# Performance work log

Hardware: AMD Instinct MI355X
Metric: run time of the kernel (lower is better)

The kernel has to match this reference:

```python
import jax, jax.numpy as jnp
import numpy as np

D_MODEL = 768
EXPAND = 2
D_STATE = 128
HEADDIM = 64
D_CONV = 4
D_INNER = EXPAND * D_MODEL            # 1536
NHEADS = D_INNER // HEADDIM           # 24
CONV_DIM = D_INNER + 2 * D_STATE      # 1792
D_IN_PROJ = 2 * D_INNER + 2 * D_STATE + NHEADS  # 3352
EPS = 1e-5
BATCH, SEQLEN = 2, 2048


def silu(v):
    return v * jax.nn.sigmoid(v)


def mamba2(x, in_w, conv_w, conv_b, dt_bias, A_log, Dp, norm_w, out_w):
    # x: (b, l, d_model)
    b, l, _ = x.shape
    zxbcdt = x @ in_w.T                              # (b, l, d_in_proj)
    z = zxbcdt[..., :D_INNER]
    xBC = zxbcdt[..., D_INNER:D_INNER + CONV_DIM]
    dt = jax.nn.softplus(zxbcdt[..., D_INNER + CONV_DIM:] + dt_bias)  # (b, l, h)
    # causal depthwise conv1d, kernel D_CONV, left padding D_CONV-1
    pad = jnp.pad(xBC, ((0, 0), (D_CONV - 1, 0), (0, 0)))
    conv = conv_b
    for k in range(D_CONV):
        conv = conv + pad[:, k:k + l, :] * conv_w[:, k]
    xBC = silu(conv)
    xh = xBC[..., :D_INNER].reshape(b, l, NHEADS, HEADDIM)   # (b,l,h,p)
    Bm = xBC[..., D_INNER:D_INNER + D_STATE]                 # (b,l,n) ngroups=1
    Cm = xBC[..., D_INNER + D_STATE:]                        # (b,l,n)
    A = -jnp.exp(A_log)                                      # (h,)
    dA = jnp.exp(dt * A)                                     # (b,l,h)

    def step(h, inp):
        dA_t, dt_t, x_t, B_t, C_t = inp
        # h: (b, h, p, n)
        h = h * dA_t[:, :, None, None] + (dt_t[:, :, None] * x_t)[..., None] * B_t[:, None, None, :]
        y = jnp.einsum('bhpn,bn->bhp', h, C_t)
        return h, y

    h0 = jnp.zeros((b, NHEADS, HEADDIM, D_STATE), x.dtype)
    xs = (dA.transpose(1, 0, 2), dt.transpose(1, 0, 2), xh.transpose(1, 0, 2, 3),
          Bm.transpose(1, 0, 2), Cm.transpose(1, 0, 2))
    _, ys = jax.lax.scan(step, h0, xs)                       # (l,b,h,p)
    y = ys.transpose(1, 0, 2, 3) + Dp[None, None, :, None] * xh
    y = y.reshape(b, l, D_INNER)
    # RMSNormGated (norm_before_gate=False): rmsnorm(y * silu(z)) * weight
    y = y * silu(z)
    y = y * jax.lax.rsqrt(jnp.mean(jnp.square(y), axis=-1, keepdims=True) + EPS) * norm_w
    return y @ out_w.T


def setup_inputs() -> dict:
    key = jax.random.key(0)
    ks = jax.random.split(key, 9)
    s = 0.02
    return {
        'x': jax.random.normal(ks[0], (BATCH, SEQLEN, D_MODEL), jnp.float32),
        'in_proj_w': jax.random.normal(ks[1], (2, D_IN_PROJ, D_MODEL), jnp.float32) * s,
        'conv_w': jax.random.normal(ks[2], (2, CONV_DIM, D_CONV), jnp.float32) * 0.2,
        'conv_b': jax.random.normal(ks[3], (2, CONV_DIM), jnp.float32) * s,
        'dt_bias': jax.random.normal(ks[4], (2, NHEADS), jnp.float32) * 0.1,
        'A_log': jnp.log(jax.random.uniform(ks[5], (2, NHEADS), jnp.float32, 1.0, 16.0)),
        'D': jax.random.normal(ks[6], (2, NHEADS), jnp.float32) * 0.5 + 1.0,
        'norm_w': jnp.ones((2, D_INNER), jnp.float32),
        'out_proj_w': jax.random.normal(ks[7], (2, D_MODEL, D_INNER), jnp.float32) * s,
    }


def reference(x, in_proj_w, conv_w, conv_b, dt_bias, A_log, D, norm_w, out_proj_w):
    h_fwd = mamba2(x, in_proj_w[0], conv_w[0], conv_b[0], dt_bias[0], A_log[0], D[0], norm_w[0], out_proj_w[0])
    x_rev = jnp.flip(x, axis=1)
    h_bwd_rev = mamba2(x_rev, in_proj_w[1], conv_w[1], conv_b[1], dt_bias[1], A_log[1], D[1], norm_w[1], out_proj_w[1])
    return h_fwd + jnp.flip(h_bwd_rev, axis=1)
```

## Files before the change

kernel.cpp:

```cpp
#include <hip/hip_runtime.h>
#include <hip/hip_bf16.h>

typedef __attribute__((ext_vector_type(8))) short short8;
typedef __attribute__((ext_vector_type(4))) short bfx4;
typedef __attribute__((ext_vector_type(4))) float floatx4;

#define SEQ     2048
#define DMODEL  768
#define DINNER  1536
#define DSTATE  128
#define NH      24
#define CONVDIM 1792
#define NPROJ   3352
#define QCH     64
#define NCH     (SEQ / QCH)

__device__ inline float bf2f(short s) {
    return __uint_as_float(((unsigned)(unsigned short)s) << 16);
}
__device__ inline short f2bf(float f) {
    __hip_bfloat16 h = __float2bfloat16(f);
    return *reinterpret_cast<short*>(&h);
}
__device__ inline void gl_lds16(const void* g, void* l) {
    __builtin_amdgcn_global_load_lds((const __attribute__((address_space(1))) unsigned int*)g,
                                     (__attribute__((address_space(3))) unsigned int*)l, 16, 0, 0);
}

__global__ __launch_bounds__(256) void cvt_kernel(const float* __restrict__ src,
                                                  __hip_bfloat16* __restrict__ dst, int n4) {
    int i = blockIdx.x * 256 + threadIdx.x;
    if (i >= n4) return;
    float4 v = *(const float4*)(src + (size_t)i * 4);
    bfx4 o = { f2bf(v.x), f2bf(v.y), f2bf(v.z), f2bf(v.w) };
    *(bfx4*)((short*)dst + (size_t)i * 4) = o;
}

__global__ __launch_bounds__(256) void gemm_bt(const __hip_bfloat16* __restrict__ Abase, size_t aStride,
                                               const __hip_bfloat16* __restrict__ Bbase, size_t bStride,
                                               float* __restrict__ C,
                                               __hip_bfloat16* __restrict__ Zb,
                                               __hip_bfloat16* __restrict__ Xb,
                                               float* __restrict__ DT,
                                               float* __restrict__ LA,
                                               const float* __restrict__ dtbias,
                                               const float* __restrict__ Alog,
                                               int M, int N, int K, int zdiv, int mode, int flipA) {
    __shared__ short As[2][64 * 64];
    __shared__ short Bs[2][64 * 64];
    int tid = threadIdx.x;
    int w = tid >> 6, lane = tid & 63;
    int q = lane >> 4, mm = lane & 15;
    int wm = w >> 1, wn = w & 1;
    int m0 = blockIdx.x * 128, n0 = blockIdx.y * 128;
    int z = blockIdx.z;
    int dir = z / zdiv, ks = z - dir * zdiv;
    int kl = K / zdiv;
    int kbeg = ks * kl;
    const short* Ag = (const short*)Abase + (size_t)dir * aStride;
    const short* Bg = (const short*)Bbase + (size_t)dir * bStride;
    int fA = flipA && dir;

    size_t aoff[2], boff[2];
    int ldso[2];
#pragma unroll
    for (int j = 0; j < 2; j++) {
        int widx = w * 2 + j;
        int ln = widx * 8 + (lane >> 3);
        int s  = lane & 7;
        int c  = s ^ (ln & 7);
        int row = (c < 4) ? ln : ln + 64;
        int ch  = (c < 4) ? c : (c ^ 4);
        int ar = m0 + row;
        if (fA) { int bb = ar >> 11, tt = ar & 2047; ar = (bb << 11) + (2047 - tt); }
        aoff[j] = (size_t)ar * K + ch * 8;
        int br = n0 + row; if (br > N - 1) br = N - 1;
        boff[j] = (size_t)br * K + ch * 8;
        ldso[j] = widx * 1024;
    }

    floatx4 acc[16];
#pragma unroll
    for (int i = 0; i < 16; i++) acc[i] = (floatx4){0.f, 0.f, 0.f, 0.f};

    int niter = kl / 32;
    auto stage = [&](int buf, int k0) {
#pragma unroll
        for (int j = 0; j < 2; j++) {
            gl_lds16(Ag + aoff[j] + kbeg + k0, (char*)&As[buf][0] + ldso[j]);
            gl_lds16(Bg + boff[j] + kbeg + k0, (char*)&Bs[buf][0] + ldso[j]);
        }
    };
    stage(0, 0);
    int slotA = (q ^ (mm & 7) ^ (wm << 2)) * 8;
    int slotB = (q ^ (mm & 7) ^ (wn << 2)) * 8;
    for (int it = 0; it < niter; it++) {
        __syncthreads();
        if (it + 1 < niter) stage((it + 1) & 1, (it + 1) * 32);
        const short* Ab = &As[it & 1][0];
        const short* Bb = &Bs[it & 1][0];
        short8 af[4], bfr[4];
#pragma unroll
        for (int mb = 0; mb < 4; mb++)
            af[mb] = *(const short8*)&Ab[(mb * 16 + mm) * 64 + slotA];
#pragma unroll
        for (int nb = 0; nb < 4; nb++)
            bfr[nb] = *(const short8*)&Bb[(nb * 16 + mm) * 64 + slotB];
#pragma unroll
        for (int mb = 0; mb < 4; mb++)
#pragma unroll
            for (int nb = 0; nb < 4; nb++)
                acc[mb * 4 + nb] = __builtin_amdgcn_mfma_f32_16x16x32_bf16(af[mb], bfr[nb], acc[mb * 4 + nb], 0, 0, 0);
    }

    __hip_bfloat16* Zb2 = Zb + (size_t)dir * 4096 * DINNER;
    __hip_bfloat16* Xb2 = Xb + (size_t)dir * 4096 * CONVDIM;
    float* DT2 = DT + (size_t)dir * 4096 * NH;
    float* LA2 = LA + (size_t)dir * 4096 * NH;
    const float* dtb2 = dtbias + dir * NH;
    const float* Al2  = Alog + dir * NH;

#pragma unroll
    for (int mb = 0; mb < 4; mb++) {
#pragma unroll
        for (int nb = 0; nb < 4; nb++) {
            int col = n0 + wn * 64 + nb * 16 + mm;
            if (col >= N) continue;
#pragma unroll
            for (int r = 0; r < 4; r++) {
                int rr = m0 + wm * 64 + mb * 16 + q * 4 + r;
                float v = acc[mb * 4 + nb][r];
                if (mode == 1) {
                    int orow = rr;
                    if (dir) { int b = rr >> 11, t = rr & 2047; orow = (b << 11) + (2047 - t); }
                    atomicAdd(&C[(size_t)orow * N + col], v);
                } else {
                    if (col < DINNER) {
                        Zb2[(size_t)rr * DINNER + col] = __float2bfloat16(v);
                    } else if (col < DINNER + CONVDIM) {
                        Xb2[(size_t)rr * CONVDIM + (col - DINNER)] = __float2bfloat16(v);
                    } else {
                        int hh = col - (DINNER + CONVDIM);
                        float raw = v + dtb2[hh];
                        float dtv = (raw > 20.f) ? raw : log1pf(__expf(raw));
                        float Av  = -__expf(Al2[hh]);
                        DT2[(size_t)rr * NH + hh] = dtv;
                        LA2[(size_t)rr * NH + hh] = dtv * Av;
                    }
                }
            }
        }
    }
}

__global__ __launch_bounds__(256) void conv_kernel(const __hip_bfloat16* __restrict__ Xb,
                                                   const float* __restrict__ conv_w,
                                                   const float* __restrict__ conv_b,
                                                   __hip_bfloat16* __restrict__ xh,
                                                   __hip_bfloat16* __restrict__ Bm,
                                                   __hip_bfloat16* __restrict__ Cm) {
    int db  = blockIdx.x >> 7;
    int dir = db >> 1;
    int t0  = (blockIdx.x & 127) * 16;
    int c8  = threadIdx.x * 8;
    if (c8 >= CONVDIM) return;

    float wk[4][8], bs[8];
#pragma unroll
    for (int j = 0; j < 8; j++) {
        bs[j] = conv_b[dir * CONVDIM + c8 + j];
#pragma unroll
        for (int k = 0; k < 4; k++) wk[k][j] = conv_w[((size_t)dir * CONVDIM + c8 + j) * 4 + k];
    }

    const short* xrow = (const short*)Xb + (size_t)db * SEQ * CONVDIM + c8;
    short8 win[4];
    const short8 zer = {0, 0, 0, 0, 0, 0, 0, 0};
#pragma unroll
    for (int k = 0; k < 3; k++) {
        int ts = t0 - 3 + k;
        win[k] = (ts >= 0) ? *(const short8*)(xrow + (size_t)ts * CONVDIM) : zer;
    }

    for (int tt = 0; tt < 16; tt++) {
        int t = t0 + tt;
        win[3] = *(const short8*)(xrow + (size_t)t * CONVDIM);
        short8 outv;
#pragma unroll
        for (int j = 0; j < 8; j++) {
            float acc = bs[j];
#pragma unroll
            for (int k = 0; k < 4; k++) acc += wk[k][j] * bf2f(win[k][j]);
            float sv = acc / (1.f + __expf(-acc));
            outv[j] = f2bf(sv);
        }
        if (c8 < DINNER)
            *(short8*)((short*)xh + (size_t)(db * SEQ + t) * DINNER + c8) = outv;
        else if (c8 < DINNER + DSTATE)
            *(short8*)((short*)Bm + (size_t)(db * SEQ + t) * DSTATE + (c8 - DINNER)) = outv;
        else
            *(short8*)((short*)Cm + (size_t)(db * SEQ + t) * DSTATE + (c8 - DINNER - DSTATE)) = outv;
        win[0] = win[1]; win[1] = win[2]; win[2] = win[3];
    }
}

__global__ __launch_bounds__(256) void ssd1_kernel(const __hip_bfloat16* __restrict__ XH,
                                                   const __hip_bfloat16* __restrict__ BMh,
                                                   const float* __restrict__ DT,
                                                   const float* __restrict__ LA,
                                                   short* __restrict__ SS,
                                                   float* __restrict__ CUM) {
    int blk = blockIdx.x;
    int ck = blk & 31;
    int dbh = blk >> 5;
    int hh = dbh % NH, db = dbh / NH;
    int base_row = db * SEQ + ck * QCH;

    __shared__ float cum_s[QCH], dt_s[QCH];
    __shared__ short Xt[64][72];
    __shared__ short Bt[128][72];

    int tid = threadIdx.x;
    int lane = tid & 63, w = tid >> 6;
    int q = lane >> 4, mm = lane & 15;

    if (tid < QCH) {
        float la  = LA[(size_t)(base_row + tid) * NH + hh];
        float dtv = DT[(size_t)(base_row + tid) * NH + hh];
        float cs = la;
#pragma unroll
        for (int d = 1; d < 64; d <<= 1) {
            float u = __shfl_up(cs, d);
            if (tid >= d) cs += u;
        }
        cum_s[tid] = cs;
        dt_s[tid] = dtv;
        CUM[(size_t)dbh * SEQ + ck * QCH + tid] = cs;
    }
    __syncthreads();
    float cumL = cum_s[QCH - 1];

    {
        int s2 = (tid & 31) * 2, pb = tid >> 5;
        float f0 = dt_s[s2]     * __expf(cumL - cum_s[s2]);
        float f1 = dt_s[s2 + 1] * __expf(cumL - cum_s[s2 + 1]);
        const short* r0 = (const short*)XH + (size_t)(base_row + s2) * DINNER + hh * 64 + pb * 8;
        const short* r1 = r0 + DINNER;
        short8 x0 = *(const short8*)r0;
        short8 x1 = *(const short8*)r1;
#pragma unroll
        for (int j = 0; j < 8; j++) {
            unsigned lo = (unsigned short)f2bf(f0 * bf2f(x0[j]));
            unsigned hi = (unsigned short)f2bf(f1 * bf2f(x1[j]));
            *(unsigned*)&Xt[pb * 8 + j][s2] = lo | (hi << 16);
        }
    }
    {
        int s2 = (tid & 31) * 2, nb = tid >> 5;
        const short* r0 = (const short*)BMh + (size_t)(base_row + s2) * DSTATE + nb * 16;
        const short* r1 = r0 + DSTATE;
        short8 b0a = *(const short8*)r0,  b0b = *(const short8*)(r0 + 8);
        short8 b1a = *(const short8*)r1,  b1b = *(const short8*)(r1 + 8);
#pragma unroll
        for (int j = 0; j < 8; j++) {
            *(unsigned*)&Bt[nb * 16 + j][s2] =
                (unsigned)(unsigned short)b0a[j] | ((unsigned)(unsigned short)b1a[j] << 16);
            *(unsigned*)&Bt[nb * 16 + 8 + j][s2] =
                (unsigned)(unsigned short)b0b[j] | ((unsigned)(unsigned short)b1b[j] << 16);
        }
    }
    __syncthreads();

    floatx4 acc[8];
#pragma unroll
    for (int i = 0; i < 8; i++) acc[i] = (floatx4){0.f, 0.f, 0.f, 0.f};
#pragma unroll
    for (int kk = 0; kk < 2; kk++) {
        short8 a = *(const short8*)&Xt[w * 16 + mm][kk * 32 + q * 8];
#pragma unroll
        for (int cb = 0; cb < 8; cb++) {
            short8 b = *(const short8*)&Bt[cb * 16 + mm][kk * 32 + q * 8];
            acc[cb] = __builtin_amdgcn_mfma_f32_16x16x32_bf16(a, b, acc[cb], 0, 0, 0);
        }
    }
    short* Sp = SS + (size_t)blk * 8192;
#pragma unroll
    for (int cb = 0; cb < 8; cb++)
#pragma unroll
        for (int r = 0; r < 4; r++)
            Sp[(w * 16 + q * 4 + r) * DSTATE + cb * 16 + mm] = f2bf(acc[cb][r]);
}

__global__ __launch_bounds__(256) void ssd2_kernel(const short* __restrict__ SS,
                                                   const float* __restrict__ CUM,
                                                   short* __restrict__ Hprev) {
    int blk = blockIdx.x;
    int dbh = blk >> 2, part = blk & 3;
    int off = part * 2048 + threadIdx.x * 8;
    size_t base = (size_t)dbh * NCH * 8192 + off;
    float h[8];
#pragma unroll
    for (int j = 0; j < 8; j++) h[j] = 0.f;
    for (int c = 0; c < NCH; c++) {
        float W = __expf(CUM[(size_t)dbh * SEQ + c * QCH + QCH - 1]);
        size_t p = base + (size_t)c * 8192;
        short8 s = *(const short8*)(SS + p);
        short8 o;
#pragma unroll
        for (int j = 0; j < 8; j++) o[j] = f2bf(h[j]);
        *(short8*)(Hprev + p) = o;
#pragma unroll
        for (int j = 0; j < 8; j++) h[j] = fmaf(h[j], W, bf2f(s[j]));
    }
}

__global__ __launch_bounds__(256) void ssd3_kernel(const __hip_bfloat16* __restrict__ XH,
                                                   const __hip_bfloat16* __restrict__ BMh,
                                                   const __hip_bfloat16* __restrict__ CMh,
                                                   const float* __restrict__ DT,
                                                   const float* __restrict__ CUM,
                                                   const short* __restrict__ Hprev,
                                                   __hip_bfloat16* __restrict__ Yb) {
    int blk = blockIdx.x;
    int ck = blk & 31;
    int dbh = blk >> 5;
    int hh = dbh % NH, db = dbh / NH;
    int base_row = db * SEQ + ck * QCH;

    __shared__ float cum_s[QCH], dt_s[QCH];
    __shared__ short Ct[64][136];
    __shared__ short G[64][72];
    __shared__ short Xt[64][72];

    int tid = threadIdx.x;
    int lane = tid & 63, w = tid >> 6;
    int q = lane >> 4, mm = lane & 15;

    if (tid < QCH) {
        cum_s[tid] = CUM[(size_t)dbh * SEQ + ck * QCH + tid];
        dt_s[tid]  = DT[(size_t)(base_row + tid) * NH + hh];
    }

    const short* Cg = (const short*)CMh + (size_t)base_row * DSTATE;
    const short* Bg = (const short*)BMh + (size_t)base_row * DSTATE;
    floatx4 P[4];
#pragma unroll
    for (int i = 0; i < 4; i++) P[i] = (floatx4){0.f, 0.f, 0.f, 0.f};
#pragma unroll
    for (int kk = 0; kk < 4; kk++) {
        short8 a = *(const short8*)(Cg + (size_t)(w * 16 + mm) * DSTATE + kk * 32 + q * 8);
#pragma unroll
        for (int cb = 0; cb < 4; cb++) {
            short8 b = *(const short8*)(Bg + (size_t)(cb * 16 + mm) * DSTATE + kk * 32 + q * 8);
            P[cb] = __builtin_amdgcn_mfma_f32_16x16x32_bf16(a, b, P[cb], 0, 0, 0);
        }
    }
    __syncthreads();

    {
        int t = tid & 63, nb4 = tid >> 6;
        float wt = __expf(cum_s[t]);
        const short* src = Cg + (size_t)t * DSTATE + nb4 * 32;
#pragma unroll
        for (int u = 0; u < 2; u++) {
            short8 v = *(const short8*)(src + u * 16);
            short8 v2 = *(const short8*)(src + u * 16 + 8);
#pragma unroll
            for (int j = 0; j < 4; j++) {
                unsigned lo = (unsigned short)f2bf(wt * bf2f(v[2 * j]));
                unsigned hi = (unsigned short)f2bf(wt * bf2f(v[2 * j + 1]));
                *(unsigned*)&Ct[t][nb4 * 32 + u * 16 + 2 * j] = lo | (hi << 16);
                lo = (unsigned short)f2bf(wt * bf2f(v2[2 * j]));
                hi = (unsigned short)f2bf(wt * bf2f(v2[2 * j + 1]));
                *(unsigned*)&Ct[t][nb4 * 32 + u * 16 + 8 + 2 * j] = lo | (hi << 16);
            }
        }
    }
    {
        int s2 = (tid & 31) * 2, pb = tid >> 5;
        const short* r0 = (const short*)XH + (size_t)(base_row + s2) * DINNER + hh * 64 + pb * 8;
        const short* r1 = r0 + DINNER;
        short8 x0 = *(const short8*)r0;
        short8 x1 = *(const short8*)r1;
#pragma unroll
        for (int j = 0; j < 8; j++) {
            *(unsigned*)&Xt[pb * 8 + j][s2] =
                (unsigned)(unsigned short)x0[j] | ((unsigned)(unsigned short)x1[j] << 16);
        }
    }
#pragma unroll
    for (int cb = 0; cb < 4; cb++) {
#pragma unroll
        for (int r = 0; r < 4; r++) {
            int t = w * 16 + q * 4 + r;
            int s = cb * 16 + mm;
            float g = (s <= t) ? P[cb][r] * __expf(cum_s[t] - cum_s[s]) * dt_s[s] : 0.f;
            G[t][s] = f2bf(g);
        }
    }
    __syncthreads();

    floatx4 Y[4];
#pragma unroll
    for (int i = 0; i < 4; i++) Y[i] = (floatx4){0.f, 0.f, 0.f, 0.f};
#pragma unroll
    for (int kk = 0; kk < 2; kk++) {
        short8 a = *(const short8*)&G[w * 16 + mm][kk * 32 + q * 8];
#pragma unroll
        for (int cb = 0; cb < 4; cb++) {
            short8 b = *(const short8*)&Xt[cb * 16 + mm][kk * 32 + q * 8];
            Y[cb] = __builtin_amdgcn_mfma_f32_16x16x32_bf16(a, b, Y[cb], 0, 0, 0);
        }
    }
    const short* Hc = Hprev + (size_t)blk * 8192;
#pragma unroll
    for (int kk = 0; kk < 4; kk++) {
        short8 a = *(const short8*)&Ct[w * 16 + mm][kk * 32 + q * 8];
#pragma unroll
        for (int cb = 0; cb < 4; cb++) {
            short8 b = *(const short8*)(Hc + (size_t)(cb * 16 + mm) * DSTATE + kk * 32 + q * 8);
            Y[cb] = __builtin_amdgcn_mfma_f32_16x16x32_bf16(a, b, Y[cb], 0, 0, 0);
        }
    }
#pragma unroll
    for (int cb = 0; cb < 4; cb++)
#pragma unroll
        for (int r = 0; r < 4; r++)
            Yb[(size_t)(base_row + w * 16 + q * 4 + r) * DINNER + hh * 64 + cb * 16 + mm] =
                __float2bfloat16(Y[cb][r]);
}

__global__ __launch_bounds__(192) void gate_kernel(const __hip_bfloat16* __restrict__ Yb,
                                                   const __hip_bfloat16* __restrict__ xh,
                                                   const __hip_bfloat16* __restrict__ Zb,
                                                   const float* __restrict__ Dp,
                                                   const float* __restrict__ norm_w,
                                                   __hip_bfloat16* __restrict__ A2) {
    int row = blockIdx.x;
    int dir = row >> 12;
    int c8 = threadIdx.x * 8;
    int hd = c8 >> 6;
    const short* yr = (const short*)Yb + (size_t)row * DINNER + c8;
    const short* xr = (const short*)xh + (size_t)row * DINNER + c8;
    const short* zr = (const short*)Zb + (size_t)row * DINNER + c8;

    short8 y8 = *(const short8*)yr;
    short8 x8 = *(const short8*)xr;
    short8 z8 = *(const short8*)zr;
    float Dv = Dp[dir * NH + hd];

    float vals[8];
    float ss = 0.f;
#pragma unroll
    for (int j = 0; j < 8; j++) {
        float v = bf2f(y8[j]) + Dv * bf2f(x8[j]);
        float z = bf2f(z8[j]);
        v *= z / (1.f + __expf(-z));
        vals[j] = v;
        ss += v * v;
    }
#pragma unroll
    for (int off = 32; off; off >>= 1) ss += __shfl_down(ss, off);
    __shared__ float ls[3];
    if ((threadIdx.x & 63) == 0) ls[threadIdx.x >> 6] = ss;
    __syncthreads();
    float tot = ls[0] + ls[1] + ls[2];
    float scale = rsqrtf(tot / (float)DINNER + 1e-5f);

    const float* nw = norm_w + dir * DINNER + c8;
    short8 o;
#pragma unroll
    for (int j = 0; j < 8; j++) o[j] = f2bf(vals[j] * scale * nw[j]);
    *(short8*)((short*)A2 + (size_t)row * DINNER + c8) = o;
}

extern "C" void kernel_launch(void* const* d_in, const int* in_sizes, int n_in,
                              void* d_out, int out_size, void* d_ws, size_t ws_size,
                              hipStream_t stream) {
    const float* x        = (const float*)d_in[0];
    const float* in_w     = (const float*)d_in[1];
    const float* conv_w   = (const float*)d_in[2];
    const float* conv_b   = (const float*)d_in[3];
    const float* dt_bias  = (const float*)d_in[4];
    const float* A_log    = (const float*)d_in[5];
    const float* Dp       = (const float*)d_in[6];
    const float* norm_w   = (const float*)d_in[7];
    const float* out_w    = (const float*)d_in[8];
    float* out = (float*)d_out;

    const size_t szW2 = (size_t)2 * DMODEL * DINNER * 2;
    const size_t szZ  = (size_t)8192 * DINNER * 2;
    const size_t szXH = (size_t)8192 * DINNER * 2;
    const size_t szBM = (size_t)8192 * DSTATE * 2;
    const size_t szCM = szBM;
    const size_t szDT = (size_t)8192 * NH * 4;
    const size_t szLA = szDT;
    const size_t szA1 = (size_t)4096 * DMODEL * 2;
    const size_t szW1 = (size_t)2 * NPROJ * DMODEL * 2;
    const size_t szXB = (size_t)8192 * CONVDIM * 2;
    const size_t szYb = (size_t)8192 * DINNER * 2;
    const size_t szSS = (size_t)96 * NCH * 8192 * 2;
    const size_t szRa = szA1 + szW1 + szXB;
    size_t szR = szRa;
    if (szR < szYb) szR = szYb;
    if (szR < szSS) szR = szSS;
    const size_t szHp = szSS;
    const size_t szCU = (size_t)96 * SEQ * 4;

    char* ws = (char*)d_ws;
    size_t off = 0;
    auto alloc = [&](size_t bytes) { char* p = ws + off; off += (bytes + 255) & ~(size_t)255; return p; };

    __hip_bfloat16* W2 = (__hip_bfloat16*)alloc(szW2);
    __hip_bfloat16* Z  = (__hip_bfloat16*)alloc(szZ);
    __hip_bfloat16* XH = (__hip_bfloat16*)alloc(szXH);
    __hip_bfloat16* BM = (__hip_bfloat16*)alloc(szBM);
    __hip_bfloat16* CM = (__hip_bfloat16*)alloc(szCM);
    float* DT = (float*)alloc(szDT);
    float* LA = (float*)alloc(szLA);
    char*  R  = (char*)alloc(szR);
    __hip_bfloat16* A1  = (__hip_bfloat16*)R;
    __hip_bfloat16* W1  = (__hip_bfloat16*)(R + szA1);
    __hip_bfloat16* XBC = (__hip_bfloat16*)(R + szA1 + szW1);
    short* SS = (short*)R;
    __hip_bfloat16* Yb = (__hip_bfloat16*)R;

    short* Hp = (short*)alloc(szHp);
    float* CU = (float*)alloc(szCU);
    if (off > ws_size) return;

    int n1 = 2 * NPROJ * DMODEL / 4;
    cvt_kernel<<<(n1 + 255) / 256, 256, 0, stream>>>(in_w, W1, n1);
    int n2 = 2 * DMODEL * DINNER / 4;
    cvt_kernel<<<(n2 + 255) / 256, 256, 0, stream>>>(out_w, W2, n2);
    int n3 = 4096 * DMODEL / 4;
    cvt_kernel<<<(n3 + 255) / 256, 256, 0, stream>>>(x, A1, n3);

    {
        dim3 grid(4096 / 128, (NPROJ + 127) / 128, 2);
        gemm_bt<<<grid, 256, 0, stream>>>(A1, 0,
                                          W1, (size_t)NPROJ * DMODEL,
                                          nullptr, Z, XBC, DT, LA, dt_bias, A_log,
                                          4096, NPROJ, DMODEL, 1, 2, 1);
    }

    conv_kernel<<<4 * 128, 256, 0, stream>>>(XBC, conv_w, conv_b, XH, BM, CM);

    ssd1_kernel<<<4 * NH * NCH, 256, 0, stream>>>(XH, BM, DT, LA, SS, CU);
    ssd2_kernel<<<4 * NH * 4, 256, 0, stream>>>(SS, CU, Hp);
    ssd3_kernel<<<4 * NH * NCH, 256, 0, stream>>>(XH, BM, CM, DT, CU, Hp, Yb);

    gate_kernel<<<2 * 4096, 192, 0, stream>>>(Yb, XH, Z, Dp, norm_w, Z);

    hipMemsetAsync(out, 0, (size_t)4096 * DMODEL * 4, stream);
    {
        dim3 grid(4096 / 128, DMODEL / 128, 4);
        gemm_bt<<<grid, 256, 0, stream>>>(Z, (size_t)4096 * DINNER,
                                          W2, (size_t)DMODEL * DINNER,
                                          out, nullptr, nullptr, nullptr, nullptr, nullptr, nullptr,
                                          4096, DMODEL, DINNER, 2, 1, 0);
    }
}
```

Baseline: 385.9 us.

## Fuse three-stage chunked SSD into one sequential-over-chunks kernel per head slice

```diff
diff --git a/kernel.cpp b/kernel.cpp
--- a/kernel.cpp
+++ b/kernel.cpp
@@ -204,230 +204,181 @@
     }
 }
 
-__global__ __launch_bounds__(256) void ssd1_kernel(const __hip_bfloat16* __restrict__ XH,
-                                                   const __hip_bfloat16* __restrict__ BMh,
-                                                   const float* __restrict__ DT,
-                                                   const float* __restrict__ LA,
-                                                   short* __restrict__ SS,
-                                                   float* __restrict__ CUM) {
+__global__ __launch_bounds__(256) void ssd_fused(const __hip_bfloat16* __restrict__ XH,
+                                                 const __hip_bfloat16* __restrict__ BMh,
+                                                 const __hip_bfloat16* __restrict__ CMh,
+                                                 const float* __restrict__ DT,
+                                                 const float* __restrict__ LA,
+                                                 __hip_bfloat16* __restrict__ Yb) {
     int blk = blockIdx.x;
-    int ck = blk & 31;
-    int dbh = blk >> 5;
+    int pg = blk & 3;
+    int dbh = blk >> 2;
     int hh = dbh % NH, db = dbh / NH;
-    int base_row = db * SEQ + ck * QCH;
+    int pbase = pg * 16;
 
     __shared__ float cum_s[QCH], dt_s[QCH];
-    __shared__ short Xt[64][72];
+    __shared__ float Wsh;
     __shared__ short Bt[128][72];
+    __shared__ short Ct[64][136];
+    __shared__ short G[64][72];
+    __shared__ short Xs[16][72];
+    __shared__ short Xu[16][72];
+    __shared__ short Hp[16][136];
 
     int tid = threadIdx.x;
     int lane = tid & 63, w = tid >> 6;
     int q = lane >> 4, mm = lane & 15;
 
-    if (tid < QCH) {
-        float la  = LA[(size_t)(base_row + tid) * NH + hh];
-        float dtv = DT[(size_t)(base_row + tid) * NH + hh];
-        float cs = la;
-#pragma unroll
-        for (int d = 1; d < 64; d <<= 1) {
-            float u = __shfl_up(cs, d);
-            if (tid >= d) cs += u;
-        }
-        cum_s[tid] = cs;
-        dt_s[tid] = dtv;
-        CUM[(size_t)dbh * SEQ + ck * QCH + tid] = cs;
-    }
-    __syncthreads();
-    float cumL = cum_s[QCH - 1];
-
-    {
-        int s2 = (tid & 31) * 2, pb = tid >> 5;
-        float f0 = dt_s[s2]     * __expf(cumL - cum_s[s2]);
-        float f1 = dt_s[s2 + 1] * __expf(cumL - cum_s[s2 + 1]);
-        const short* r0 = (const short*)XH + (size_t)(base_row + s2) * DINNER + hh * 64 + pb * 8;
-        const short* r1 = r0 + DINNER;
-        short8 x0 = *(const short8*)r0;
-        short8 x1 = *(const short8*)r1;
-#pragma unroll
-        for (int j = 0; j < 8; j++) {
-            unsigned lo = (unsigned short)f2bf(f0 * bf2f(x0[j]));
-            unsigned hi = (unsigned short)f2bf(f1 * bf2f(x1[j]));
-            *(unsigned*)&Xt[pb * 8 + j][s2] = lo | (hi << 16);
-        }
-    }
-    {
-        int s2 = (tid & 31) * 2, nb = tid >> 5;
-        const short* r0 = (const short*)BMh + (size_t)(base_row + s2) * DSTATE + nb * 16;
-        const short* r1 = r0 + DSTATE;
-        short8 b0a = *(const short8*)r0,  b0b = *(const short8*)(r0 + 8);
-        short8 b1a = *(const short8*)r1,  b1b = *(const short8*)(r1 + 8);
-#pragma unroll
-        for (int j = 0; j < 8; j++) {
-            *(unsigned*)&Bt[nb * 16 + j][s2] =
-                (unsigned)(unsigned short)b0a[j] | ((unsigned)(unsigned short)b1a[j] << 16);
-            *(unsigned*)&Bt[nb * 16 + 8 + j][s2] =
-                (unsigned)(unsigned short)b0b[j] | ((unsigned)(unsigned short)b1b[j] << 16);
-        }
-    }
-    __syncthreads();
-
-    floatx4 acc[8];
-#pragma unroll
-    for (int i = 0; i < 8; i++) acc[i] = (floatx4){0.f, 0.f, 0.f, 0.f};
-#pragma unroll
-    for (int kk = 0; kk < 2; kk++) {
-        short8 a = *(const short8*)&Xt[w * 16 + mm][kk * 32 + q * 8];
-#pragma unroll
-        for (int cb = 0; cb < 8; cb++) {
-            short8 b = *(const short8*)&Bt[cb * 16 + mm][kk * 32 + q * 8];
-            acc[cb] = __builtin_amdgcn_mfma_f32_16x16x32_bf16(a, b, acc[cb], 0, 0, 0);
-        }
-    }
-    short* Sp = SS + (size_t)blk * 8192;
-#pragma unroll
-    for (int cb = 0; cb < 8; cb++)
+    float h[2][4];
+#pragma unroll
+    for (int a = 0; a < 2; a++)
+#pragma unroll
+        for (int r = 0; r < 4; r++) h[a][r] = 0.f;
+
+    for (int ck = 0; ck < NCH; ck++) {
+        int base_row = db * SEQ + ck * QCH;
+        const short* Cg = (const short*)CMh + (size_t)base_row * DSTATE;
+        const short* Bg = (const short*)BMh + (size_t)base_row * DSTATE;
+
+        if (tid < QCH) {
+            float la  = LA[(size_t)(base_row + tid) * NH + hh];
+            float dtv = DT[(size_t)(base_row + tid) * NH + hh];
+            float cs = la;
+#pragma unroll
+            for (int d = 1; d < 64; d <<= 1) {
+                float u = __shfl_up(cs, d);
+                if (tid >= d) cs += u;
+            }
+            cum_s[tid] = cs;
+            dt_s[tid]  = dtv;
+            if (tid == QCH - 1) Wsh = __expf(cs);
+        }
+
+        floatx4 P[4];
+#pragma unroll
+        for (int i = 0; i < 4; i++) P[i] = (floatx4){0.f, 0.f, 0.f, 0.f};
+#pragma unroll
+        for (int kk = 0; kk < 4; kk++) {
+            short8 a = *(const short8*)(Cg + (size_t)(w * 16 + mm) * DSTATE + kk * 32 + q * 8);
+#pragma unroll
+            for (int cb = 0; cb < 4; cb++) {
+                short8 b = *(const short8*)(Bg + (size_t)(cb * 16 + mm) * DSTATE + kk * 32 + q * 8);
+                P[cb] = __builtin_amdgcn_mfma_f32_16x16x32_bf16(a, b, P[cb], 0, 0, 0);
+            }
+        }
+        __syncthreads();
+
+        {
+            int t = tid & 63, nb4 = tid >> 6;
+            float wt = __expf(cum_s[t]);
+            const short* src = Cg + (size_t)t * DSTATE + nb4 * 32;
+#pragma unroll
+            for (int u = 0; u < 2; u++) {
+                short8 v  = *(const short8*)(src + u * 16);
+                short8 v2 = *(const short8*)(src + u * 16 + 8);
+#pragma unroll
+                for (int j = 0; j < 4; j++) {
+                    unsigned lo = (unsigned short)f2bf(wt * bf2f(v[2 * j]));
+                    unsigned hi = (unsigned short)f2bf(wt * bf2f(v[2 * j + 1]));
+                    *(unsigned*)&Ct[t][nb4 * 32 + u * 16 + 2 * j] = lo | (hi << 16);
+                    lo = (unsigned short)f2bf(wt * bf2f(v2[2 * j]));
+                    hi = (unsigned short)f2bf(wt * bf2f(v2[2 * j + 1]));
+                    *(unsigned*)&Ct[t][nb4 * 32 + u * 16 + 8 + 2 * j] = lo | (hi << 16);
+                }
+            }
+        }
+        {
+            int s2 = (tid & 31) * 2, nb = tid >> 5;
+            const short* r0 = Bg + (size_t)s2 * DSTATE + nb * 16;
+            const short* r1 = r0 + DSTATE;
+            short8 b0a = *(const short8*)r0,  b0b = *(const short8*)(r0 + 8);
+            short8 b1a = *(const short8*)r1,  b1b = *(const short8*)(r1 + 8);
+#pragma unroll
+            for (int j = 0; j < 8; j++) {
+                *(unsigned*)&Bt[nb * 16 + j][s2] =
+                    (unsigned)(unsigned short)b0a[j] | ((unsigned)(unsigned short)b1a[j] << 16);
+                *(unsigned*)&Bt[nb * 16 + 8 + j][s2] =
+                    (unsigned)(unsigned short)b0b[j] | ((unsigned)(unsigned short)b1b[j] << 16);
+            }
+        }
+        if (tid < 128) {
+            int s2 = (tid & 31) * 2;
+            int pb = (tid >> 5) & 1;
+            const short* r0 = (const short*)XH + (size_t)(base_row + s2) * DINNER + hh * 64 + pbase + pb * 8;
+            const short* r1 = r0 + DINNER;
+            short8 x0 = *(const short8*)r0;
+            short8 x1 = *(const short8*)r1;
+            if (tid >= 64) {
+                float f0 = dt_s[s2]     * __expf(cum_s[QCH - 1] - cum_s[s2]);
+                float f1 = dt_s[s2 + 1] * __expf(cum_s[QCH - 1] - cum_s[s2 + 1]);
+#pragma unroll
+                for (int j = 0; j < 8; j++) {
+                    unsigned lo = (unsigned short)f2bf(f0 * bf2f(x0[j]));
+                    unsigned hi = (unsigned short)f2bf(f1 * bf2f(x1[j]));
+                    *(unsigned*)&Xs[pb * 8 + j][s2] = lo | (hi << 16);
+                }
+            } else {
+#pragma unroll
+                for (int j = 0; j < 8; j++) {
+                    *(unsigned*)&Xu[pb * 8 + j][s2] =
+                        (unsigned)(unsigned short)x0[j] | ((unsigned)(unsigned short)x1[j] << 16);
+                }
+            }
+        }
+#pragma unroll
+        for (int cb = 0; cb < 4; cb++) {
+#pragma unroll
+            for (int r = 0; r < 4; r++) {
+                int t = w * 16 + q * 4 + r;
+                int s = cb * 16 + mm;
+                float g = (s <= t) ? P[cb][r] * __expf(cum_s[t] - cum_s[s]) * dt_s[s] : 0.f;
+                G[t][s] = f2bf(g);
+            }
+        }
+#pragma unroll
+        for (int a = 0; a < 2; a++)
+#pragma unroll
+            for (int r = 0; r < 4; r++)
+                Hp[q * 4 + r][(w * 2 + a) * 16 + mm] = f2bf(h[a][r]);
+        __syncthreads();
+
+        floatx4 Sa[2];
+        Sa[0] = (floatx4){0.f, 0.f, 0.f, 0.f};
+        Sa[1] = (floatx4){0.f, 0.f, 0.f, 0.f};
+#pragma unroll
+        for (int kk = 0; kk < 2; kk++) {
+            short8 a = *(const short8*)&Xs[mm][kk * 32 + q * 8];
+#pragma unroll
+            for (int nb2 = 0; nb2 < 2; nb2++) {
+                short8 b = *(const short8*)&Bt[(w * 2 + nb2) * 16 + mm][kk * 32 + q * 8];
+                Sa[nb2] = __builtin_amdgcn_mfma_f32_16x16x32_bf16(a, b, Sa[nb2], 0, 0, 0);
+            }
+        }
+        floatx4 Y = (floatx4){0.f, 0.f, 0.f, 0.f};
+#pragma unroll
+        for (int kk = 0; kk < 2; kk++) {
+            short8 a = *(const short8*)&G[w * 16 + mm][kk * 32 + q * 8];
+            short8 b = *(const short8*)&Xu[mm][kk * 32 + q * 8];
+            Y = __builtin_amdgcn_mfma_f32_16x16x32_bf16(a, b, Y, 0, 0, 0);
+        }
+#pragma unroll
+        for (int kk = 0; kk < 4; kk++) {
+            short8 a = *(const short8*)&Ct[w * 16 + mm][kk * 32 + q * 8];
+            short8 b = *(const short8*)&Hp[mm][kk * 32 + q * 8];
+            Y = __builtin_amdgcn_mfma_f32_16x16x32_bf16(a, b, Y, 0, 0, 0);
+        }
+        float Wv = Wsh;
+#pragma unroll
+        for (int a = 0; a < 2; a++)
+#pragma unroll
+            for (int r = 0; r < 4; r++)
+                h[a][r] = fmaf(h[a][r], Wv, Sa[a][r]);
 #pragma unroll
         for (int r = 0; r < 4; r++)
-            Sp[(w * 16 + q * 4 + r) * DSTATE + cb * 16 + mm] = f2bf(acc[cb][r]);
-}
-
-__global__ __launch_bounds__(256) void ssd2_kernel(const short* __restrict__ SS,
-                                                   const float* __restrict__ CUM,
-                                                   short* __restrict__ Hprev) {
-    int blk = blockIdx.x;
-    int dbh = blk >> 2, part = blk & 3;
-    int off = part * 2048 + threadIdx.x * 8;
-    size_t base = (size_t)dbh * NCH * 8192 + off;
-    float h[8];
-#pragma unroll
-    for (int j = 0; j < 8; j++) h[j] = 0.f;
-    for (int c = 0; c < NCH; c++) {
-        float W = __expf(CUM[(size_t)dbh * SEQ + c * QCH + QCH - 1]);
-        size_t p = base + (size_t)c * 8192;
-        short8 s = *(const short8*)(SS + p);
-        short8 o;
-#pragma unroll
-        for (int j = 0; j < 8; j++) o[j] = f2bf(h[j]);
-        *(short8*)(Hprev + p) = o;
-#pragma unroll
-        for (int j = 0; j < 8; j++) h[j] = fmaf(h[j], W, bf2f(s[j]));
-    }
-}
-
-__global__ __launch_bounds__(256) void ssd3_kernel(const __hip_bfloat16* __restrict__ XH,
-                                                   const __hip_bfloat16* __restrict__ BMh,
-                                                   const __hip_bfloat16* __restrict__ CMh,
-                                                   const float* __restrict__ DT,
-                                                   const float* __restrict__ CUM,
-                                                   const short* __restrict__ Hprev,
-                                                   __hip_bfloat16* __restrict__ Yb) {
-    int blk = blockIdx.x;
-    int ck = blk & 31;
-    int dbh = blk >> 5;
-    int hh = dbh % NH, db = dbh / NH;
-    int base_row = db * SEQ + ck * QCH;
-
-    __shared__ float cum_s[QCH], dt_s[QCH];
-    __shared__ short Ct[64][136];
-    __shared__ short G[64][72];
-    __shared__ short Xt[64][72];
-
-    int tid = threadIdx.x;
-    int lane = tid & 63, w = tid >> 6;
-    int q = lane >> 4, mm = lane & 15;
-
-    if (tid < QCH) {
-        cum_s[tid] = CUM[(size_t)dbh * SEQ + ck * QCH + tid];
-        dt_s[tid]  = DT[(size_t)(base_row + tid) * NH + hh];
-    }
-
-    const short* Cg = (const short*)CMh + (size_t)base_row * DSTATE;
-    const short* Bg = (const short*)BMh + (size_t)base_row * DSTATE;
-    floatx4 P[4];
-#pragma unroll
-    for (int i = 0; i < 4; i++) P[i] = (floatx4){0.f, 0.f, 0.f, 0.f};
-#pragma unroll
-    for (int kk = 0; kk < 4; kk++) {
-        short8 a = *(const short8*)(Cg + (size_t)(w * 16 + mm) * DSTATE + kk * 32 + q * 8);
-#pragma unroll
-        for (int cb = 0; cb < 4; cb++) {
-            short8 b = *(const short8*)(Bg + (size_t)(cb * 16 + mm) * DSTATE + kk * 32 + q * 8);
-            P[cb] = __builtin_amdgcn_mfma_f32_16x16x32_bf16(a, b, P[cb], 0, 0, 0);
-        }
-    }
-    __syncthreads();
-
-    {
-        int t = tid & 63, nb4 = tid >> 6;
-        float wt = __expf(cum_s[t]);
-        const short* src = Cg + (size_t)t * DSTATE + nb4 * 32;
-#pragma unroll
-        for (int u = 0; u < 2; u++) {
-            short8 v = *(const short8*)(src + u * 16);
-            short8 v2 = *(const short8*)(src + u * 16 + 8);
-#pragma unroll
-            for (int j = 0; j < 4; j++) {
-                unsigned lo = (unsigned short)f2bf(wt * bf2f(v[2 * j]));
-                unsigned hi = (unsigned short)f2bf(wt * bf2f(v[2 * j + 1]));
-                *(unsigned*)&Ct[t][nb4 * 32 + u * 16 + 2 * j] = lo | (hi << 16);
-                lo = (unsigned short)f2bf(wt * bf2f(v2[2 * j]));
-                hi = (unsigned short)f2bf(wt * bf2f(v2[2 * j + 1]));
-                *(unsigned*)&Ct[t][nb4 * 32 + u * 16 + 8 + 2 * j] = lo | (hi << 16);
-            }
-        }
-    }
-    {
-        int s2 = (tid & 31) * 2, pb = tid >> 5;
-        const short* r0 = (const short*)XH + (size_t)(base_row + s2) * DINNER + hh * 64 + pb * 8;
-        const short* r1 = r0 + DINNER;
-        short8 x0 = *(const short8*)r0;
-        short8 x1 = *(const short8*)r1;
-#pragma unroll
-        for (int j = 0; j < 8; j++) {
-            *(unsigned*)&Xt[pb * 8 + j][s2] =
-                (unsigned)(unsigned short)x0[j] | ((unsigned)(unsigned short)x1[j] << 16);
-        }
-    }
-#pragma unroll
-    for (int cb = 0; cb < 4; cb++) {
-#pragma unroll
-        for (int r = 0; r < 4; r++) {
-            int t = w * 16 + q * 4 + r;
-            int s = cb * 16 + mm;
-            float g = (s <= t) ? P[cb][r] * __expf(cum_s[t] - cum_s[s]) * dt_s[s] : 0.f;
-            G[t][s] = f2bf(g);
-        }
-    }
-    __syncthreads();
-
-    floatx4 Y[4];
-#pragma unroll
-    for (int i = 0; i < 4; i++) Y[i] = (floatx4){0.f, 0.f, 0.f, 0.f};
-#pragma unroll
-    for (int kk = 0; kk < 2; kk++) {
-        short8 a = *(const short8*)&G[w * 16 + mm][kk * 32 + q * 8];
-#pragma unroll
-        for (int cb = 0; cb < 4; cb++) {
-            short8 b = *(const short8*)&Xt[cb * 16 + mm][kk * 32 + q * 8];
-            Y[cb] = __builtin_amdgcn_mfma_f32_16x16x32_bf16(a, b, Y[cb], 0, 0, 0);
-        }
-    }
-    const short* Hc = Hprev + (size_t)blk * 8192;
-#pragma unroll
-    for (int kk = 0; kk < 4; kk++) {
-        short8 a = *(const short8*)&Ct[w * 16 + mm][kk * 32 + q * 8];
-#pragma unroll
-        for (int cb = 0; cb < 4; cb++) {
-            short8 b = *(const short8*)(Hc + (size_t)(cb * 16 + mm) * DSTATE + kk * 32 + q * 8);
-            Y[cb] = __builtin_amdgcn_mfma_f32_16x16x32_bf16(a, b, Y[cb], 0, 0, 0);
-        }
-    }
-#pragma unroll
-    for (int cb = 0; cb < 4; cb++)
-#pragma unroll
-        for (int r = 0; r < 4; r++)
-            Yb[(size_t)(base_row + w * 16 + q * 4 + r) * DINNER + hh * 64 + cb * 16 + mm] =
-                __float2bfloat16(Y[cb][r]);
+            Yb[(size_t)(base_row + w * 16 + q * 4 + r) * DINNER + hh * 64 + pbase + mm] =
+                __float2bfloat16(Y[r]);
+        __syncthreads();
+    }
 }
 
 __global__ __launch_bounds__(192) void gate_kernel(const __hip_bfloat16* __restrict__ Yb,
@@ -499,13 +450,8 @@
     const size_t szW1 = (size_t)2 * NPROJ * DMODEL * 2;
     const size_t szXB = (size_t)8192 * CONVDIM * 2;
     const size_t szYb = (size_t)8192 * DINNER * 2;
-    const size_t szSS = (size_t)96 * NCH * 8192 * 2;
     const size_t szRa = szA1 + szW1 + szXB;
-    size_t szR = szRa;
-    if (szR < szYb) szR = szYb;
-    if (szR < szSS) szR = szSS;
-    const size_t szHp = szSS;
-    const size_t szCU = (size_t)96 * SEQ * 4;
+    size_t szR = (szRa > szYb) ? szRa : szYb;
 
     char* ws = (char*)d_ws;
     size_t off = 0;
@@ -522,11 +468,7 @@
     __hip_bfloat16* A1  = (__hip_bfloat16*)R;
     __hip_bfloat16* W1  = (__hip_bfloat16*)(R + szA1);
     __hip_bfloat16* XBC = (__hip_bfloat16*)(R + szA1 + szW1);
-    short* SS = (short*)R;
     __hip_bfloat16* Yb = (__hip_bfloat16*)R;
-
-    short* Hp = (short*)alloc(szHp);
-    float* CU = (float*)alloc(szCU);
     if (off > ws_size) return;
 
     int n1 = 2 * NPROJ * DMODEL / 4;
@@ -546,9 +488,7 @@
 
     conv_kernel<<<4 * 128, 256, 0, stream>>>(XBC, conv_w, conv_b, XH, BM, CM);
 
-    ssd1_kernel<<<4 * NH * NCH, 256, 0, stream>>>(XH, BM, DT, LA, SS, CU);
-    ssd2_kernel<<<4 * NH * 4, 256, 0, stream>>>(SS, CU, Hp);
-    ssd3_kernel<<<4 * NH * NCH, 256, 0, stream>>>(XH, BM, CM, DT, CU, Hp, Yb);
+    ssd_fused<<<4 * NH * 4, 256, 0, stream>>>(XH, BM, CM, DT, LA, Yb);
 
     gate_kernel<<<2 * 4096, 192, 0, stream>>>(Yb, XH, Z, Dp, norm_w, Z);
 
```

Result: slower. 526.8 us (+36.5%).
